# Optimization experiments

Measured on AMD Instinct MI355X. Metric: run time of the kernel, lower is better.

The kernel has to match this reference:

```python
import jax, jax.numpy as jnp
import numpy as np

# Dims: B latent vectors processed through T sequential LALR-state calls.
B, T = 4096, 128      # batch of latent vecs, timesteps
NL = 256              # n_latent (scaled up from default 100)
NS = 64               # number of LALR states with learned layers
NO = 32               # output tokens per state (Linear(n_latent, n_out))
V = 64                # len(terminals): size of scattered output vector


def setup_inputs() -> dict:
    key = jax.random.key(0)
    ks = jax.random.split(key, 7)
    return {
        "latent0": jax.random.normal(ks[0], (B, NL), jnp.float32),
        "W1": jax.random.normal(ks[1], (NS, NL, NL), jnp.float32) / np.sqrt(NL).astype(np.float32),
        "b1": jax.random.normal(ks[2], (NS, NL), jnp.float32) * 0.01,
        "W2": jax.random.normal(ks[3], (NS, NO, NL), jnp.float32) / np.sqrt(NL).astype(np.float32),
        "b2": jax.random.normal(ks[4], (NS, NO), jnp.float32) * 0.01,
        "state_seq": jax.random.randint(ks[5], (T,), 0, NS, jnp.int32),
        "out_idx": jax.random.randint(ks[6], (NS, NO), 0, V, jnp.int32),
    }


def reference(latent0, W1, b1, W2, b2, state_seq, out_idx):
    """Per-timestep LALR state call:
       newlatent = tanh(Linear(x));
       probs     = softmax(Linear(newlatent));
       output    = IndicesExpansion: scatter probs into zeros(V) at out_idx[state].
    State weights are gathered by state id; batch is processed jointly."""
    def step(x, s):
        w1, bb1 = W1[s], b1[s]            # [NL,NL], [NL]
        w2, bb2 = W2[s], b2[s]            # [NO,NL], [NO]
        idx = out_idx[s]                  # [NO]
        x_new = jnp.tanh(x @ w1.T + bb1)                       # [B, NL]
        probs = jax.nn.softmax(x_new @ w2.T + bb2, axis=-1)    # [B, NO]
        # IndicesExpansionLayer: zero vector of size V, set vals at indices
        y = jnp.zeros((x.shape[0], V), x.dtype).at[:, idx].set(probs)
        return x_new, y

    final_latent, ys = jax.lax.scan(step, latent0, state_seq)  # ys: [T, B, V]
    return jnp.transpose(ys, (1, 0, 2))  # [B, T, V]
```

## Files before the change

### kernel.cpp

```cpp
#include <hip/hip_runtime.h>

#define B_  4096
#define T_  128
#define NL  256
#define NS  64
#define NO  32
#define V_  64
#define RB  16
#define NBLK (B_ / RB)

typedef __bf16 bf16;
typedef bf16  bf16x8 __attribute__((ext_vector_type(8)));
typedef bf16  bf16x4 __attribute__((ext_vector_type(4)));
typedef float f32x4  __attribute__((ext_vector_type(4)));

#define MF(a, b, c) __builtin_amdgcn_mfma_f32_16x16x32_bf16(a, b, c, 0, 0, 0)

#define LGKM_BARRIER() asm volatile("s_waitcnt lgkmcnt(0)\n\ts_barrier" ::: "memory")

#define GLOAD(dst, ptr) \
    asm volatile("global_load_dwordx4 %0, %1, off" : "=v"(dst) : "v"(ptr))

template <int TSHIFT>
__global__ void split_w_frag(const float* __restrict__ src,
                             bf16* __restrict__ hi, bf16* __restrict__ lo,
                             int total4) {
    int t4 = blockIdx.x * blockDim.x + threadIdx.x;
    if (t4 >= total4) return;
    const int jb   = (t4 & 1) * 4;
    const int L    = (t4 >> 1) & 63;
    const int ks   = (t4 >> 7) & 7;
    const int rest = t4 >> 10;
    const int t    = rest & ((1 << TSHIFT) - 1);
    const int s    = rest >> TSHIFT;
    const int row  = ((s << TSHIFT) + t) * 16 + (L & 15);
    const int k    = ks * 32 + (L >> 4) * 8 + jb;
    const float4 v = *(const float4*)(src + (size_t)row * NL + k);
    float vv[4] = {v.x, v.y, v.z, v.w};
    bf16x4 h, l;
#pragma unroll
    for (int e = 0; e < 4; e++) {
        bf16 hh = (bf16)vv[e];
        h[e] = hh;
        l[e] = (bf16)(vv[e] - (float)hh);
    }
    *(bf16x4*)(hi + (size_t)t4 * 4) = h;
    *(bf16x4*)(lo + (size_t)t4 * 4) = l;
}

__global__ void inv_kernel(const int* __restrict__ out_idx, int* __restrict__ inv) {
    int t = blockIdx.x * blockDim.x + threadIdx.x;
    if (t >= NS * V_) return;
    int s = t >> 6, v = t & 63;
    int jf = -1;
#pragma unroll
    for (int j = 0; j < NO; j++)
        if (out_idx[(s << 5) | j] == v) jf = j;
    inv[t] = jf;
}

__device__ __forceinline__ float fast_tanh(float z) {
    float e = __expf(2.0f * z);
    return 1.0f - 2.0f / (e + 1.0f);
}

__device__ __forceinline__ int xaddr(int t, int q, int n) {
    return ((t >> 1) * 512) + (((t & 1) * 2 + (q >> 1)) * 128) + n * 8 + (q & 1) * 4;
}

__launch_bounds__(1024, 4)
__global__ void lalr_main(const float* __restrict__ latent0,
                          const float* __restrict__ b1,
                          const float* __restrict__ b2,
                          const int*   __restrict__ state_seq,
                          const int*   __restrict__ inv,
                          const bf16*  __restrict__ W1h, const bf16* __restrict__ W1l,
                          const bf16*  __restrict__ W2h, const bf16* __restrict__ W2l,
                          float* __restrict__ out) {
    __shared__ bf16  xh[2][4096];
    __shared__ bf16  xl[2][4096];
    __shared__ float Sp[2][8][16][36];
    __shared__ float b1s[NS * NL];
    __shared__ float b2s[NS * NO];
    __shared__ int   invs[NS * V_];
    __shared__ int   sseq[T_];

    const int tid  = threadIdx.x;
    const int wave = tid >> 6;
    const int lane = tid & 63;
    const int n    = lane & 15;
    const int q    = lane >> 4;
    const int r0   = blockIdx.x * RB;
    const int t2   = wave & 1;
    const int ks2  = wave >> 1;

    const int rot = (blockIdx.x >> 3) & 7;
    const int d0 = ((0 + rot) & 7) * 512;
    const int d1 = ((1 + rot) & 7) * 512;
    const int d2 = ((2 + rot) & 7) * 512;
    const int d3 = ((3 + rot) & 7) * 512;
    const int d4 = ((4 + rot) & 7) * 512;
    const int d5 = ((5 + rot) & 7) * 512;
    const int d6 = ((6 + rot) & 7) * 512;
    const int d7 = ((7 + rot) & 7) * 512;

    for (int k = tid; k < NS * NL / 4; k += 1024)
        ((float4*)b1s)[k] = ((const float4*)b1)[k];
    if (tid < NS * NO / 4) ((float4*)b2s)[tid] = ((const float4*)b2)[tid];
    if (tid < NS * V_ / 4) ((int4*)invs)[tid] = ((const int4*)inv)[tid];
    if (tid < T_) sseq[tid] = state_seq[tid];

    {
        float4 v = *(const float4*)(latent0 + (size_t)(r0 + n) * NL + wave * 16 + q * 4);
        float vv[4] = {v.x, v.y, v.z, v.w};
        bf16x4 hv, lv;
#pragma unroll
        for (int e = 0; e < 4; e++) {
            bf16 hh = (bf16)vv[e];
            hv[e] = hh;
            lv[e] = (bf16)(vv[e] - (float)hh);
        }
        const int a = xaddr(wave, q, n);
        *(bf16x4*)(&xh[0][a]) = hv;
        *(bf16x4*)(&xl[0][a]) = lv;
    }

    int s0 = state_seq[0], s1 = -1, s2 = -1;

    bf16x8 pwh0, pwh1, pwh2, pwh3, pwh4, pwh5, pwh6, pwh7;
    bf16x8 pwl0, pwl1, pwl2, pwl3, pwl4, pwl5, pwl6, pwl7;
    bf16x8 w2h2, w2l2;

    const size_t wfrag = (size_t)wave * 8 * 512 + lane * 8;

    {
        const bf16* h0 = W1h + (size_t)s0 * 16 * 8 * 512 + wfrag;
        const bf16* l0 = W1l + (size_t)s0 * 16 * 8 * 512 + wfrag;
        GLOAD(pwh0, h0 + d0); GLOAD(pwl0, l0 + d0);
        GLOAD(pwh1, h0 + d1); GLOAD(pwl1, l0 + d1);
        GLOAD(pwh2, h0 + d2); GLOAD(pwl2, l0 + d2);
        GLOAD(pwh3, h0 + d3); GLOAD(pwl3, l0 + d3);
        GLOAD(pwh4, h0 + d4); GLOAD(pwl4, l0 + d4);
        GLOAD(pwh5, h0 + d5); GLOAD(pwl5, l0 + d5);
        GLOAD(pwh6, h0 + d6); GLOAD(pwl6, l0 + d6);
        GLOAD(pwh7, h0 + d7); GLOAD(pwl7, l0 + d7);
        const bf16* c2h = W2h + (size_t)((s0 * 2 + t2) * 8 + ks2) * 512 + lane * 8;
        const bf16* c2l = W2l + (size_t)((s0 * 2 + t2) * 8 + ks2) * 512 + lane * 8;
        GLOAD(w2h2, c2h);     GLOAD(w2l2, c2l);
    }

    LGKM_BARRIER();

#define G1S(ks, dks) {                                                      \
        bf16x8 xa = *(const bf16x8*)(&xh[cur][dks + lane * 8]);             \
        bf16x8 xb = *(const bf16x8*)(&xl[cur][dks + lane * 8]);             \
        asm volatile("s_waitcnt vmcnt(16)" ::: "memory");                   \
        __builtin_amdgcn_sched_barrier(0);                                  \
        acc1 = MF(pwh##ks, xa, acc1);                                       \
        acc1 = MF(pwl##ks, xa, acc1);                                       \
        acc1 = MF(pwh##ks, xb, acc1);                                       \
        GLOAD(pwh##ks, nh0 + dks);                                          \
        GLOAD(pwl##ks, nl0 + dks);                                          \
    }

    for (int i = 0; i <= T_ + 1; i++) {
        const int ib  = i & 1;
        const int cur = ib;

        const int ns0 = (i + 1 < T_) ? sseq[i + 1] : -1;
        const int ls  = (ns0 >= 0) ? ns0 : 0;
        const bf16* nh0 = W1h + (size_t)ls * 16 * 8 * 512 + wfrag;
        const bf16* nl0 = W1l + (size_t)ls * 16 * 8 * 512 + wfrag;

        f32x4 acc1;
        if (s0 >= 0) {
            acc1 = (f32x4){0.f, 0.f, 0.f, 0.f};
            G1S(0, d0)
            G1S(1, d1)
            G1S(2, d2)
            G1S(3, d3)
            G1S(4, d4)
            G1S(5, d5)
            G1S(6, d6)
            G1S(7, d7)
        }

        if (s1 >= 0) {
            bf16x8 xa = *(const bf16x8*)(&xh[cur][ks2 * 512 + lane * 8]);
            bf16x8 xb = *(const bf16x8*)(&xl[cur][ks2 * 512 + lane * 8]);
            if (s0 >= 0) {
                asm volatile("s_waitcnt vmcnt(16)" ::: "memory");
            } else {
                asm volatile("s_waitcnt vmcnt(0)" ::: "memory");
            }
            __builtin_amdgcn_sched_barrier(0);
            f32x4 a2 = (f32x4){0.f, 0.f, 0.f, 0.f};
            a2 = MF(w2h2, xa, a2);
            a2 = MF(w2l2, xa, a2);
            a2 = MF(w2h2, xb, a2);
            if (ks2 == 0) {
                float4 bb = *(const float4*)(&b2s[s1 * NO + t2 * 16 + q * 4]);
                a2[0] += bb.x; a2[1] += bb.y; a2[2] += bb.z; a2[3] += bb.w;
            }
            *(f32x4*)(&Sp[ib][ks2][n][t2 * 16 + q * 4]) = a2;
        }
        if (s0 >= 0) {
            const bf16* n2h = W2h + (size_t)((s0 * 2 + t2) * 8 + ks2) * 512 + lane * 8;
            const bf16* n2l = W2l + (size_t)((s0 * 2 + t2) * 8 + ks2) * 512 + lane * 8;
            GLOAD(w2h2, n2h);
            GLOAD(w2l2, n2l);
        }

        if (s2 >= 0 && tid < 256) {
            const int r  = tid >> 4;
            const int j0 = tid & 15;
            const int pb = (i - 1) & 1;
            float v0 = 0.f, v1 = 0.f;
#pragma unroll
            for (int w = 0; w < 8; w++) {
                v0 += Sp[pb][w][r][j0];
                v1 += Sp[pb][w][r][j0 + 16];
            }
            float m = fmaxf(v0, v1);
#pragma unroll
            for (int d = 1; d < 16; d <<= 1) m = fmaxf(m, __shfl_xor(m, d));
            float e0 = __expf(v0 - m), e1 = __expf(v1 - m);
            float su = e0 + e1;
#pragma unroll
            for (int d = 1; d < 16; d <<= 1) su += __shfl_xor(su, d);
            float is = 1.0f / su;
            float p0 = e0 * is, p1 = e1 * is;
            const int gb = lane & 48;
            int4 iv4 = *(const int4*)(&invs[s2 * V_ + j0 * 4]);
            int ivv[4] = {iv4.x, iv4.y, iv4.z, iv4.w};
            float o[4];
#pragma unroll
            for (int e = 0; e < 4; e++) {
                float ga = __shfl(p0, gb + (ivv[e] & 15));
                float gc = __shfl(p1, gb + (ivv[e] & 15));
                o[e] = (ivv[e] < 0) ? 0.f : ((ivv[e] < 16) ? ga : gc);
            }
            *(float4*)(out + ((size_t)(r0 + r) * T_ + (i - 2)) * V_ + j0 * 4) = *(float4*)o;
        }

        if (s0 >= 0) {
            float4 bb = *(const float4*)(&b1s[s0 * NL + wave * 16 + q * 4]);
            float bv[4] = {bb.x, bb.y, bb.z, bb.w};
            bf16x4 hv, lv;
#pragma unroll
            for (int e = 0; e < 4; e++) {
                float h = fast_tanh(acc1[e] + bv[e]);
                bf16 hh = (bf16)h;
                hv[e] = hh;
                lv[e] = (bf16)(h - (float)hh);
            }
            const int a = xaddr(wave, q, n);
            *(bf16x4*)(&xh[cur ^ 1][a]) = hv;
            *(bf16x4*)(&xl[cur ^ 1][a]) = lv;
        }

        s2 = s1; s1 = s0; s0 = ns0;
        LGKM_BARRIER();
    }
#undef G1S
}

extern "C" void kernel_launch(void* const* d_in, const int* in_sizes, int n_in,
                              void* d_out, int out_size, void* d_ws, size_t ws_size,
                              hipStream_t stream) {
    const float* latent0   = (const float*)d_in[0];
    const float* W1        = (const float*)d_in[1];
    const float* b1        = (const float*)d_in[2];
    const float* W2        = (const float*)d_in[3];
    const float* b2        = (const float*)d_in[4];
    const int*   state_seq = (const int*)d_in[5];
    const int*   out_idx   = (const int*)d_in[6];
    float* out = (float*)d_out;

    bf16* W1h = (bf16*)d_ws;
    bf16* W1l = W1h + (size_t)NS * NL * NL;
    bf16* W2h = W1l + (size_t)NS * NL * NL;
    bf16* W2l = W2h + (size_t)NS * NO * NL;
    int*  inv = (int*)(W2l + (size_t)NS * NO * NL);

    const int n4_w1 = NS * NL * NL / 4;
    const int n4_w2 = NS * NO * NL / 4;
    split_w_frag<4><<<n4_w1 / 256, 256, 0, stream>>>(W1, W1h, W1l, n4_w1);
    split_w_frag<1><<<n4_w2 / 256, 256, 0, stream>>>(W2, W2h, W2l, n4_w2);
    inv_kernel<<<(NS * V_ + 255) / 256, 256, 0, stream>>>(out_idx, inv);

    lalr_main<<<NBLK, 1024, 0, stream>>>(latent0, b1, b2, state_seq, inv,
                                         W1h, W1l, W2h, W2l, out);
}
```

Baseline: 535.6 us.

## Switch split weights to fp16 high part plus int8-quantized low residual

Moves the three-term split-precision MFMA scheme from bf16 to fp16 and stores the low residual of each weight as a signed int8 with a fixed 2^-20 scale instead of a full bf16. This cuts the per-step weight bytes streamed from global memory by about a quarter. The int8 residuals are unpacked back to fp16 in registers before the MFMA. The cost is extra VALU unpack work on the critical path, plus a risk of accuracy loss if weights exceed fp16 range or residuals saturate the int8 clamp.

```diff
diff --git a/kernel.cpp b/kernel.cpp
--- a/kernel.cpp
+++ b/kernel.cpp
@@ -9,21 +9,24 @@
 #define RB  16
 #define NBLK (B_ / RB)
 
-typedef __bf16 bf16;
-typedef bf16  bf16x8 __attribute__((ext_vector_type(8)));
-typedef bf16  bf16x4 __attribute__((ext_vector_type(4)));
-typedef float f32x4  __attribute__((ext_vector_type(4)));
-
-#define MF(a, b, c) __builtin_amdgcn_mfma_f32_16x16x32_bf16(a, b, c, 0, 0, 0)
+typedef _Float16 f16;
+typedef f16   f16x8 __attribute__((ext_vector_type(8)));
+typedef f16   f16x4 __attribute__((ext_vector_type(4)));
+typedef int   ix2   __attribute__((ext_vector_type(2)));
+typedef float f32x4 __attribute__((ext_vector_type(4)));
+
+#define MF(a, b, c) __builtin_amdgcn_mfma_f32_16x16x32_f16(a, b, c, 0, 0, 0)
 
 #define LGKM_BARRIER() asm volatile("s_waitcnt lgkmcnt(0)\n\ts_barrier" ::: "memory")
 
-#define GLOAD(dst, ptr) \
+#define GLOAD4(dst, ptr) \
     asm volatile("global_load_dwordx4 %0, %1, off" : "=v"(dst) : "v"(ptr))
+#define GLOADQ(dst, ptr) \
+    asm volatile("global_load_dwordx2 %0, %1, off" : "=v"(dst) : "v"(ptr))
 
 template <int TSHIFT>
 __global__ void split_w_frag(const float* __restrict__ src,
-                             bf16* __restrict__ hi, bf16* __restrict__ lo,
+                             f16* __restrict__ hi, char* __restrict__ qlo,
                              int total4) {
     int t4 = blockIdx.x * blockDim.x + threadIdx.x;
     if (t4 >= total4) return;
@@ -37,15 +40,18 @@
     const int k    = ks * 32 + (L >> 4) * 8 + jb;
     const float4 v = *(const float4*)(src + (size_t)row * NL + k);
     float vv[4] = {v.x, v.y, v.z, v.w};
-    bf16x4 h, l;
+    f16x4 h;
+    int qb = 0;
 #pragma unroll
     for (int e = 0; e < 4; e++) {
-        bf16 hh = (bf16)vv[e];
+        f16 hh = (f16)vv[e];
         h[e] = hh;
-        l[e] = (bf16)(vv[e] - (float)hh);
-    }
-    *(bf16x4*)(hi + (size_t)t4 * 4) = h;
-    *(bf16x4*)(lo + (size_t)t4 * 4) = l;
+        float lo = vv[e] - (float)hh;
+        float qf = fminf(fmaxf(rintf(lo * 0x1p20f), -127.f), 127.f);
+        qb |= (((int)qf) & 0xff) << (8 * e);
+    }
+    *(f16x4*)(hi + (size_t)t4 * 4) = h;
+    ((int*)qlo)[t4] = qb;
 }
 
 __global__ void inv_kernel(const int* __restrict__ out_idx, int* __restrict__ inv) {
@@ -62,6 +68,18 @@
 __device__ __forceinline__ float fast_tanh(float z) {
     float e = __expf(2.0f * z);
     return 1.0f - 2.0f / (e + 1.0f);
+}
+
+__device__ __forceinline__ f16x8 unpack_q(ix2 qd) {
+    f16x8 r;
+#pragma unroll
+    for (int j = 0; j < 4; j++) {
+        int b0 = (int)(signed char)((qd[0] >> (8 * j)) & 0xff);
+        int b1 = (int)(signed char)((qd[1] >> (8 * j)) & 0xff);
+        r[j]     = (f16)((float)b0 * 0x1p-20f);
+        r[j + 4] = (f16)((float)b1 * 0x1p-20f);
+    }
+    return r;
 }
 
 __device__ __forceinline__ int xaddr(int t, int q, int n) {
@@ -74,11 +92,11 @@
                           const float* __restrict__ b2,
                           const int*   __restrict__ state_seq,
                           const int*   __restrict__ inv,
-                          const bf16*  __restrict__ W1h, const bf16* __restrict__ W1l,
-                          const bf16*  __restrict__ W2h, const bf16* __restrict__ W2l,
+                          const f16*   __restrict__ W1F, const char* __restrict__ W1Q,
+                          const f16*   __restrict__ W2F, const char* __restrict__ W2Q,
                           float* __restrict__ out) {
-    __shared__ bf16  xh[2][4096];
-    __shared__ bf16  xl[2][4096];
+    __shared__ f16   xh[2][4096];
+    __shared__ f16   xl[2][4096];
     __shared__ float Sp[2][8][16][36];
     __shared__ float b1s[NS * NL];
     __shared__ float b2s[NS * NO];
@@ -95,14 +113,9 @@
     const int ks2  = wave >> 1;
 
     const int rot = (blockIdx.x >> 3) & 7;
-    const int d0 = ((0 + rot) & 7) * 512;
-    const int d1 = ((1 + rot) & 7) * 512;
-    const int d2 = ((2 + rot) & 7) * 512;
-    const int d3 = ((3 + rot) & 7) * 512;
-    const int d4 = ((4 + rot) & 7) * 512;
-    const int d5 = ((5 + rot) & 7) * 512;
-    const int d6 = ((6 + rot) & 7) * 512;
-    const int d7 = ((7 + rot) & 7) * 512;
+    const int rs0 = (0 + rot) & 7, rs1 = (1 + rot) & 7, rs2 = (2 + rot) & 7,
+              rs3 = (3 + rot) & 7, rs4 = (4 + rot) & 7, rs5 = (5 + rot) & 7,
+              rs6 = (6 + rot) & 7, rs7 = (7 + rot) & 7;
 
     for (int k = tid; k < NS * NL / 4; k += 1024)
         ((float4*)b1s)[k] = ((const float4*)b1)[k];
@@ -113,54 +126,58 @@
     {
         float4 v = *(const float4*)(latent0 + (size_t)(r0 + n) * NL + wave * 16 + q * 4);
         float vv[4] = {v.x, v.y, v.z, v.w};
-        bf16x4 hv, lv;
+        f16x4 hv, lv;
 #pragma unroll
         for (int e = 0; e < 4; e++) {
-            bf16 hh = (bf16)vv[e];
+            f16 hh = (f16)vv[e];
             hv[e] = hh;
-            lv[e] = (bf16)(vv[e] - (float)hh);
+            lv[e] = (f16)(vv[e] - (float)hh);
         }
         const int a = xaddr(wave, q, n);
-        *(bf16x4*)(&xh[0][a]) = hv;
-        *(bf16x4*)(&xl[0][a]) = lv;
+        *(f16x4*)(&xh[0][a]) = hv;
+        *(f16x4*)(&xl[0][a]) = lv;
     }
 
     int s0 = state_seq[0], s1 = -1, s2 = -1;
 
-    bf16x8 pwh0, pwh1, pwh2, pwh3, pwh4, pwh5, pwh6, pwh7;
-    bf16x8 pwl0, pwl1, pwl2, pwl3, pwl4, pwl5, pwl6, pwl7;
-    bf16x8 w2h2, w2l2;
-
-    const size_t wfrag = (size_t)wave * 8 * 512 + lane * 8;
+    f16x8 pwh0, pwh1, pwh2, pwh3, pwh4, pwh5, pwh6, pwh7;
+    ix2   pwq0, pwq1, pwq2, pwq3, pwq4, pwq5, pwq6, pwq7;
+    f16x8 w2h2;
+    ix2   w2q2;
+
+    const int wfrag = wave * 4096 + lane * 8;
 
     {
-        const bf16* h0 = W1h + (size_t)s0 * 16 * 8 * 512 + wfrag;
-        const bf16* l0 = W1l + (size_t)s0 * 16 * 8 * 512 + wfrag;
-        GLOAD(pwh0, h0 + d0); GLOAD(pwl0, l0 + d0);
-        GLOAD(pwh1, h0 + d1); GLOAD(pwl1, l0 + d1);
-        GLOAD(pwh2, h0 + d2); GLOAD(pwl2, l0 + d2);
-        GLOAD(pwh3, h0 + d3); GLOAD(pwl3, l0 + d3);
-        GLOAD(pwh4, h0 + d4); GLOAD(pwl4, l0 + d4);
-        GLOAD(pwh5, h0 + d5); GLOAD(pwl5, l0 + d5);
-        GLOAD(pwh6, h0 + d6); GLOAD(pwl6, l0 + d6);
-        GLOAD(pwh7, h0 + d7); GLOAD(pwl7, l0 + d7);
-        const bf16* c2h = W2h + (size_t)((s0 * 2 + t2) * 8 + ks2) * 512 + lane * 8;
-        const bf16* c2l = W2l + (size_t)((s0 * 2 + t2) * 8 + ks2) * 512 + lane * 8;
-        GLOAD(w2h2, c2h);     GLOAD(w2l2, c2l);
+        const f16*  h0 = W1F + (size_t)s0 * 65536 + wfrag;
+        const char* q0 = W1Q + (size_t)s0 * 65536 + wfrag;
+        GLOAD4(pwh0, h0 + rs0 * 512); GLOADQ(pwq0, q0 + rs0 * 512);
+        GLOAD4(pwh1, h0 + rs1 * 512); GLOADQ(pwq1, q0 + rs1 * 512);
+        GLOAD4(pwh2, h0 + rs2 * 512); GLOADQ(pwq2, q0 + rs2 * 512);
+        GLOAD4(pwh3, h0 + rs3 * 512); GLOADQ(pwq3, q0 + rs3 * 512);
+        GLOAD4(pwh4, h0 + rs4 * 512); GLOADQ(pwq4, q0 + rs4 * 512);
+        GLOAD4(pwh5, h0 + rs5 * 512); GLOADQ(pwq5, q0 + rs5 * 512);
+        GLOAD4(pwh6, h0 + rs6 * 512); GLOADQ(pwq6, q0 + rs6 * 512);
+        GLOAD4(pwh7, h0 + rs7 * 512); GLOADQ(pwq7, q0 + rs7 * 512);
+        const f16*  c2h = W2F + (size_t)((s0 * 2 + t2) * 8 + ks2) * 512 + lane * 8;
+        const char* c2q = W2Q + (size_t)((s0 * 2 + t2) * 8 + ks2) * 512 + lane * 8;
+        GLOAD4(w2h2, c2h); GLOADQ(w2q2, c2q);
     }
 
     LGKM_BARRIER();
 
-#define G1S(ks, dks) {                                                      \
-        bf16x8 xa = *(const bf16x8*)(&xh[cur][dks + lane * 8]);             \
-        bf16x8 xb = *(const bf16x8*)(&xl[cur][dks + lane * 8]);             \
-        asm volatile("s_waitcnt vmcnt(16)" ::: "memory");                   \
+#define G1S(ks, rs) {                                                       \
+        const int xo = (rs) * 512 + lane * 8;                               \
+        f16x8 xa = *(const f16x8*)(&xh[cur][xo]);                           \
+        f16x8 xb = *(const f16x8*)(&xl[cur][xo]);                           \
+        asm volatile("s_waitcnt vmcnt(16)"                                  \
+                     : "+v"(pwh##ks), "+v"(pwq##ks) :: "memory");           \
         __builtin_amdgcn_sched_barrier(0);                                  \
         acc1 = MF(pwh##ks, xa, acc1);                                       \
-        acc1 = MF(pwl##ks, xa, acc1);                                       \
+        f16x8 wl = unpack_q(pwq##ks);                                       \
+        acc1 = MF(wl, xa, acc1);                                            \
         acc1 = MF(pwh##ks, xb, acc1);                                       \
-        GLOAD(pwh##ks, nh0 + dks);                                          \
-        GLOAD(pwl##ks, nl0 + dks);                                          \
+        GLOAD4(pwh##ks, nh0 + (rs) * 512);                                  \
+        GLOADQ(pwq##ks, nq0 + (rs) * 512);                                  \
     }
 
     for (int i = 0; i <= T_ + 1; i++) {
@@ -169,34 +186,38 @@
 
         const int ns0 = (i + 1 < T_) ? sseq[i + 1] : -1;
         const int ls  = (ns0 >= 0) ? ns0 : 0;
-        const bf16* nh0 = W1h + (size_t)ls * 16 * 8 * 512 + wfrag;
-        const bf16* nl0 = W1l + (size_t)ls * 16 * 8 * 512 + wfrag;
+        const f16*  nh0 = W1F + (size_t)ls * 65536 + wfrag;
+        const char* nq0 = W1Q + (size_t)ls * 65536 + wfrag;
 
         f32x4 acc1;
         if (s0 >= 0) {
             acc1 = (f32x4){0.f, 0.f, 0.f, 0.f};
-            G1S(0, d0)
-            G1S(1, d1)
-            G1S(2, d2)
-            G1S(3, d3)
-            G1S(4, d4)
-            G1S(5, d5)
-            G1S(6, d6)
-            G1S(7, d7)
+            G1S(0, rs0)
+            G1S(1, rs1)
+            G1S(2, rs2)
+            G1S(3, rs3)
+            G1S(4, rs4)
+            G1S(5, rs5)
+            G1S(6, rs6)
+            G1S(7, rs7)
         }
 
         if (s1 >= 0) {
-            bf16x8 xa = *(const bf16x8*)(&xh[cur][ks2 * 512 + lane * 8]);
-            bf16x8 xb = *(const bf16x8*)(&xl[cur][ks2 * 512 + lane * 8]);
+            const int xo2 = ks2 * 512 + lane * 8;
+            f16x8 xa = *(const f16x8*)(&xh[cur][xo2]);
+            f16x8 xb = *(const f16x8*)(&xl[cur][xo2]);
             if (s0 >= 0) {
-                asm volatile("s_waitcnt vmcnt(16)" ::: "memory");
+                asm volatile("s_waitcnt vmcnt(16)"
+                             : "+v"(w2h2), "+v"(w2q2) :: "memory");
             } else {
-                asm volatile("s_waitcnt vmcnt(0)" ::: "memory");
+                asm volatile("s_waitcnt vmcnt(0)"
+                             : "+v"(w2h2), "+v"(w2q2) :: "memory");
             }
             __builtin_amdgcn_sched_barrier(0);
             f32x4 a2 = (f32x4){0.f, 0.f, 0.f, 0.f};
             a2 = MF(w2h2, xa, a2);
-            a2 = MF(w2l2, xa, a2);
+            f16x8 wl2 = unpack_q(w2q2);
+            a2 = MF(wl2, xa, a2);
             a2 = MF(w2h2, xb, a2);
             if (ks2 == 0) {
                 float4 bb = *(const float4*)(&b2s[s1 * NO + t2 * 16 + q * 4]);
@@ -205,10 +226,10 @@
             *(f32x4*)(&Sp[ib][ks2][n][t2 * 16 + q * 4]) = a2;
         }
         if (s0 >= 0) {
-            const bf16* n2h = W2h + (size_t)((s0 * 2 + t2) * 8 + ks2) * 512 + lane * 8;
-            const bf16* n2l = W2l + (size_t)((s0 * 2 + t2) * 8 + ks2) * 512 + lane * 8;
-            GLOAD(w2h2, n2h);
-            GLOAD(w2l2, n2l);
+            const f16*  n2h = W2F + (size_t)((s0 * 2 + t2) * 8 + ks2) * 512 + lane * 8;
+            const char* n2q = W2Q + (size_t)((s0 * 2 + t2) * 8 + ks2) * 512 + lane * 8;
+            GLOAD4(w2h2, n2h);
+            GLOADQ(w2q2, n2q);
         }
 
         if (s2 >= 0 && tid < 256) {
@@ -246,17 +267,17 @@
         if (s0 >= 0) {
             float4 bb = *(const float4*)(&b1s[s0 * NL + wave * 16 + q * 4]);
             float bv[4] = {bb.x, bb.y, bb.z, bb.w};
-            bf16x4 hv, lv;
+            f16x4 hv, lv;
 #pragma unroll
             for (int e = 0; e < 4; e++) {
                 float h = fast_tanh(acc1[e] + bv[e]);
-                bf16 hh = (bf16)h;
+                f16 hh = (f16)h;
                 hv[e] = hh;
-                lv[e] = (bf16)(h - (float)hh);
+                lv[e] = (f16)(h - (float)hh);
             }
             const int a = xaddr(wave, q, n);
-            *(bf16x4*)(&xh[cur ^ 1][a]) = hv;
-            *(bf16x4*)(&xl[cur ^ 1][a]) = lv;
+            *(f16x4*)(&xh[cur ^ 1][a]) = hv;
+            *(f16x4*)(&xl[cur ^ 1][a]) = lv;
         }
 
         s2 = s1; s1 = s0; s0 = ns0;
@@ -277,18 +298,18 @@
     const int*   out_idx   = (const int*)d_in[6];
     float* out = (float*)d_out;
 
-    bf16* W1h = (bf16*)d_ws;
-    bf16* W1l = W1h + (size_t)NS * NL * NL;
-    bf16* W2h = W1l + (size_t)NS * NL * NL;
-    bf16* W2l = W2h + (size_t)NS * NO * NL;
-    int*  inv = (int*)(W2l + (size_t)NS * NO * NL);
+    f16*  W1F = (f16*)d_ws;
+    char* W1Q = (char*)(W1F + (size_t)NS * NL * NL);
+    f16*  W2F = (f16*)(W1Q + (size_t)NS * NL * NL);
+    char* W2Q = (char*)(W2F + (size_t)NS * NO * NL);
+    int*  inv = (int*)(W2Q + (size_t)NS * NO * NL);
 
     const int n4_w1 = NS * NL * NL / 4;
     const int n4_w2 = NS * NO * NL / 4;
-    split_w_frag<4><<<n4_w1 / 256, 256, 0, stream>>>(W1, W1h, W1l, n4_w1);
-    split_w_frag<1><<<n4_w2 / 256, 256, 0, stream>>>(W2, W2h, W2l, n4_w2);
+    split_w_frag<4><<<n4_w1 / 256, 256, 0, stream>>>(W1, W1F, W1Q, n4_w1);
+    split_w_frag<1><<<n4_w2 / 256, 256, 0, stream>>>(W2, W2F, W2Q, n4_w2);
     inv_kernel<<<(NS * V_ + 255) / 256, 256, 0, stream>>>(out_idx, inv);
 
     lalr_main<<<NBLK, 1024, 0, stream>>>(latent0, b1, b2, state_seq, inv,
-                                         W1h, W1l, W2h, W2l, out);
-}
+                                         W1F, W1Q, W2F, W2Q, out);
+}
```

Measured after the change: 574.1 us. 1.07x slower.
